# Optimization experiments

Measured on AMD Instinct MI355X. Metric: run time of the kernel, lower is better.

## Reference

```python
import jax, jax.numpy as jnp
import numpy as np

# Straight-through deterministic binarization (sign), identity grad —
# matches the .data in-place Binarize trick in BinaryNet.pytorch.
@jax.custom_vjp
def binarize(x):
    return jnp.sign(x)
def _bin_fwd(x):
    return jnp.sign(x), None
def _bin_bwd(res, g):
    return (g,)
binarize.defvjp(_bin_fwd, _bin_bwd)

# Stochastic binary activation: p = hard_sigmoid(x), out = 2*Bernoulli(p)-1,
# straight-through estimator gated on |x|<=1.
@jax.custom_vjp
def stoch_act(x, u):
    p = jnp.clip((x + 1.0) * 0.5, 0.0, 1.0)
    return jnp.where(u < p, 1.0, -1.0).astype(x.dtype)
def _sa_fwd(x, u):
    p = jnp.clip((x + 1.0) * 0.5, 0.0, 1.0)
    return jnp.where(u < p, 1.0, -1.0).astype(x.dtype), x
def _sa_bwd(x, g):
    return (g * (jnp.abs(x) <= 1.0).astype(g.dtype), jnp.zeros(x.shape, g.dtype))
stoch_act.defvjp(_sa_fwd, _sa_bwd)

def bconv(x, w, b, bin_in):
    # BinarizeConv2d: binarize input unless it has 3 channels; always binarize weight
    xi = binarize(x) if bin_in else x
    y = jax.lax.conv_general_dilated(
        xi, binarize(w), window_strides=(1, 1), padding=((1, 1), (1, 1)),
        dimension_numbers=('NCHW', 'OIHW', 'NCHW'))
    return y + b[None, :, None, None]

def blin(x, w, b):
    # BinarizeLinear: input dim != 784 so input is binarized; weight binarized
    return binarize(x) @ binarize(w).T + b

def _forward(x, w1, b1, w2, b2, w3, b3, w4, b4, w5, b5, w6, b6, fw1, fb1, fw2, fb2, fw3, fb3):
    keys = jax.random.split(jax.random.key(42), 9)
    def act(h, i):
        return stoch_act(h, jax.random.uniform(keys[i], h.shape, h.dtype))
    h = act(bconv(x, w1, b1, False), 0)          # [B,128,32,32]
    h = act(bconv(h, w2, b2, True), 1)           # [B,256,32,32]
    h = act(bconv(h, w3, b3, True), 2)
    h = act(bconv(h, w4, b4, True), 3)
    h = act(bconv(h, w5, b5, True), 4)           # [B,512,32,32]
    h = act(bconv(h, w6, b6, True), 5)
    h = h.reshape(-1, 512 * 4 * 4)               # faithful view(-1, 8192) -> [64*B, 8192]
    h = act(blin(h, fw1, fb1), 6)
    h = act(blin(h, fw2, fb2), 7)
    h = act(blin(h, fw3, fb3), 8)                # [64*B, 10]
    return h

def setup_inputs():
    key = jax.random.key(0)
    ks = jax.random.split(key, 20)
    n = lambda k, s: jax.random.normal(k, s, jnp.float32)
    return {
        'x': n(ks[0], (64, 3, 32, 32)),
        'w1': n(ks[1], (128, 3, 3, 3)) * 0.1, 'b1': n(ks[2], (128,)) * 0.1,
        'w2': n(ks[3], (256, 128, 3, 3)) * 0.1, 'b2': n(ks[4], (256,)) * 0.1,
        'w3': n(ks[5], (256, 256, 3, 3)) * 0.1, 'b3': n(ks[6], (256,)) * 0.1,
        'w4': n(ks[7], (256, 256, 3, 3)) * 0.1, 'b4': n(ks[8], (256,)) * 0.1,
        'w5': n(ks[9], (512, 256, 3, 3)) * 0.1, 'b5': n(ks[10], (512,)) * 0.1,
        'w6': n(ks[11], (512, 512, 3, 3)) * 0.1, 'b6': n(ks[12], (512,)) * 0.1,
        'fw1': n(ks[13], (1024, 8192)) * 0.02, 'fb1': n(ks[14], (1024,)) * 0.02,
        'fw2': n(ks[15], (1024, 1024)) * 0.02, 'fb2': n(ks[16], (1024,)) * 0.02,
        'fw3': n(ks[17], (10, 1024)) * 0.02, 'fb3': n(ks[18], (10,)) * 0.02,
    }

def reference(x, w1, b1, w2, b2, w3, b3, w4, b4, w5, b5, w6, b6, fw1, fb1, fw2, fb2, fw3, fb3):
    return _forward(x, w1, b1, w2, b2, w3, b3, w4, b4, w5, b5, w6, b6, fw1, fb1, fw2, fb2, fw3, fb3)
```

## Files before the change

### kernel.cpp

```cpp
#include <hip/hip_runtime.h>
#include <stdint.h>

typedef unsigned int u32;
typedef unsigned long long u64;
typedef int v4i __attribute__((ext_vector_type(4)));
typedef int v16i __attribute__((ext_vector_type(16)));

__host__ __device__ __forceinline__ void tf2x32(u32 k0, u32 k1, u32 x0, u32 x1,
                                                u32& o0, u32& o1) {
  u32 k2 = k0 ^ k1 ^ 0x1BD11BDAu;
  x0 += k0; x1 += k1;
#ifdef __HIP_DEVICE_COMPILE__
#define ROTL(v, r) __builtin_rotateleft32((v), (r))
#else
#define ROTL(v, r) (((v) << (r)) | ((v) >> (32 - (r))))
#endif
#define TFR(r) { x0 += x1; x1 = ROTL(x1, r); x1 ^= x0; }
  TFR(13) TFR(15) TFR(26) TFR(6)   x0 += k1; x1 += k2 + 1u;
  TFR(17) TFR(29) TFR(16) TFR(24)  x0 += k2; x1 += k0 + 2u;
  TFR(13) TFR(15) TFR(26) TFR(6)   x0 += k0; x1 += k1 + 3u;
  TFR(17) TFR(29) TFR(16) TFR(24)  x0 += k1; x1 += k2 + 4u;
  TFR(13) TFR(15) TFR(26) TFR(6)   x0 += k2; x1 += k0 + 5u;
#undef TFR
#undef ROTL
  o0 = x0; o1 = x1;
}

__device__ __forceinline__ bool act_neg(float y, u32 k0, u32 k1, u32 j) {
  u32 o0, o1;
  tf2x32(k0, k1, 0u, j, o0, o1);
  u32 bits = o0 ^ o1;
  float uf = __uint_as_float(0x3f800000u | (bits >> 9));
  float u2 = __builtin_fmaf(uf, 2.0f, -2.0f);
  float t1 = y + 1.0f;
  return !(u2 < t1);
}

__global__ void k_pack_wfrag(const float* __restrict__ w, u32* __restrict__ bf,
                             int Cout, int Cin) {
  const int W = Cin >> 5;
  const int total = (Cout >> 5) * W * 9 * 256;
  int idx = blockIdx.x * blockDim.x + threadIdx.x;
  if (idx >= total) return;
  int i4 = idx & 3;
  int l = (idx >> 2) & 63;
  int t = (idx >> 8) % 9;
  int kt = (idx / 2304) % W;
  int cot = idx / (2304 * W);
  int co = cot * 32 + (l & 31);
  int ci0 = kt * 32 + (l >> 5) * 16 + i4 * 4;
  int kh = t / 3, kw = t % 3;
  u32 v = 0;
#pragma unroll
  for (int b = 0; b < 4; ++b) {
    float wf = w[((size_t)(co * Cin + ci0 + b) * 3 + kh) * 3 + kw];
    v |= (wf < 0.0f ? 0xFFu : 0x01u) << (8 * b);
  }
  bf[idx] = v;
}

__global__ void k_pack_fcwT(const float* __restrict__ w, u32* __restrict__ pwT,
                            int O, int K) {
  int KW = K >> 5;
  int idx = blockIdx.x * blockDim.x + threadIdx.x;
  if (idx >= O * KW) return;
  int kw = idx % KW, o = idx / KW;
  const float4* src = (const float4*)(w + (size_t)o * K + kw * 32);
  u32 word = 0;
#pragma unroll
  for (int b4 = 0; b4 < 8; ++b4) {
    float4 f = src[b4];
    word |= (f.x < 0.0f ? 1u : 0u) << (b4 * 4 + 0);
    word |= (f.y < 0.0f ? 1u : 0u) << (b4 * 4 + 1);
    word |= (f.z < 0.0f ? 1u : 0u) << (b4 * 4 + 2);
    word |= (f.w < 0.0f ? 1u : 0u) << (b4 * 4 + 3);
  }
  int k4 = kw >> 2, j = kw & 3;
  pwT[((size_t)k4 * O + o) * 4 + j] = word;
}

__global__ void k_pack_fcw(const float* __restrict__ w, u32* __restrict__ pw,
                           int O, int K) {
  int KW = K >> 5;
  int idx = blockIdx.x * blockDim.x + threadIdx.x;
  if (idx >= O * KW) return;
  int kw = idx % KW, o = idx / KW;
  const float4* src = (const float4*)(w + (size_t)o * K + kw * 32);
  u32 word = 0;
#pragma unroll
  for (int b4 = 0; b4 < 8; ++b4) {
    float4 f = src[b4];
    word |= (f.x < 0.0f ? 1u : 0u) << (b4 * 4 + 0);
    word |= (f.y < 0.0f ? 1u : 0u) << (b4 * 4 + 1);
    word |= (f.z < 0.0f ? 1u : 0u) << (b4 * 4 + 2);
    word |= (f.w < 0.0f ? 1u : 0u) << (b4 * 4 + 3);
  }
  pw[idx] = word;
}

__global__ __launch_bounds__(256) void k_conv1(
    const float* __restrict__ x, const float* __restrict__ w1,
    const float* __restrict__ b1, u32 k0, u32 k1, u32* __restrict__ out) {
  int wave = (blockIdx.x * 256 + threadIdx.x) >> 6;
  int lane = threadIdx.x & 63;
  int n = wave >> 10;
  int rem = wave & 1023;
  int y = rem >> 5, xx = rem & 31;

  float xv[27];
#pragma unroll
  for (int ci = 0; ci < 3; ++ci)
#pragma unroll
    for (int dy = -1; dy <= 1; ++dy)
#pragma unroll
      for (int dx = -1; dx <= 1; ++dx) {
        int gy = y + dy, gx = xx + dx;
        float v = 0.0f;
        if ((unsigned)gy < 32u && (unsigned)gx < 32u)
          v = x[((n * 3 + ci) * 32 + gy) * 32 + gx];
        xv[(ci * 3 + (dy + 1)) * 3 + (dx + 1)] = v;
      }

  u64 bm[2];
#pragma unroll
  for (int h = 0; h < 2; ++h) {
    int co = lane + h * 64;
    float acc = 0.0f;
#pragma unroll
    for (int kh = 0; kh < 3; ++kh)
#pragma unroll
      for (int kw = 0; kw < 3; ++kw)
#pragma unroll
        for (int ci = 0; ci < 3; ++ci) {
          int k = (ci * 3 + kh) * 3 + kw;
          float wv = w1[co * 27 + k];
          acc += (wv < 0.0f) ? -xv[k] : xv[k];
        }
    float yv = acc + b1[co];
    u32 j = ((u32)(n * 128 + co) << 10) | (u32)(y << 5) | (u32)xx;
    bm[h] = __ballot(act_neg(yv, k0, k1, j));
  }
  if (lane < 4) {
    u32 wsel = (lane & 1) ? (u32)(bm[lane >> 1] >> 32) : (u32)bm[lane >> 1];
    out[(u32)(n * 4 + lane) * 1024u + (u32)(y * 32 + xx)] = wsel;
  }
}

template <int W>
__global__ __launch_bounds__(512) void k_bconv11(
    const u32* __restrict__ in, const u32* __restrict__ bfrag,
    const float* __restrict__ bias, int Cout, u32 k0, u32 k1,
    u32* __restrict__ out) {
  const int tid = threadIdx.x;
  const int lane = tid & 63;
  const int wv = tid >> 6;
  const int n = blockIdx.x;
  const int y0 = blockIdx.y * 4;
  const int cot = blockIdx.z * 8 + wv;
  const int WOUT = Cout >> 5;

  __shared__ __align__(16) u32 sl[2][2][6 * 36 * 4];

  const int er = tid / 34;
  const int exc = tid % 34;
  const bool eact = tid < 204;
  const int egy = y0 - 1 + er;
  const int egx = exc - 1;
  const bool ein =
      eact && ((unsigned)egy < 32u) && ((unsigned)egx < 32u);

  v16i acc[4];
#pragma unroll
  for (int r = 0; r < 4; ++r)
#pragma unroll
    for (int e = 0; e < 16; ++e) acc[r][e] = 0;

  {
    u32 word = ein ? in[(u32)(n * W) * 1024u + (u32)(egy * 32 + egx)] : 0u;
    if (eact) {
#pragma unroll
      for (int h = 0; h < 2; ++h) {
        v4i v;
#pragma unroll
        for (int q = 0; q < 4; ++q) {
          u32 nib = (word >> ((4 * h + q) * 4)) & 0xFu;
          u32 spread = (nib * 0x00204081u) & 0x01010101u;
          u32 val = (spread * 0xFEu) ^ 0x01010101u;
          v[q] = ein ? (int)val : 0;
        }
        *(v4i*)&sl[0][h][(er * 36 + exc) * 4] = v;
      }
    }
  }
  __syncthreads();

#pragma unroll 1
  for (int kt = 0; kt < W; ++kt) {
    const int cur = kt & 1;
    u32 wn = 0;
    if (kt + 1 < W && ein)
      wn = in[(u32)(n * W + kt + 1) * 1024u + (u32)(egy * 32 + egx)];

    v4i af[18];
    const int xb = lane & 31;
    const u32* slc = sl[cur][lane >> 5];
#pragma unroll
    for (int sr = 0; sr < 6; ++sr)
#pragma unroll
      for (int dxx = 0; dxx < 3; ++dxx)
        af[sr * 3 + dxx] = *(const v4i*)&slc[(sr * 36 + xb + dxx) * 4];

    const u32* bptr = bfrag + ((size_t)(cot * W + kt) * 9) * 256 + lane * 4;
#pragma unroll
    for (int t = 0; t < 9; ++t) {
      v4i B = *(const v4i*)(bptr + t * 256);
      const int dy = t / 3 - 1, dxx = t % 3;
#pragma unroll
      for (int r = 0; r < 4; ++r)
        acc[r] = __builtin_amdgcn_mfma_i32_32x32x32_i8(
            af[(r + dy + 1) * 3 + dxx], B, acc[r], 0, 0, 0);
    }

    if (kt + 1 < W && eact) {
#pragma unroll
      for (int h = 0; h < 2; ++h) {
        v4i v;
#pragma unroll
        for (int q = 0; q < 4; ++q) {
          u32 nib = (wn >> ((4 * h + q) * 4)) & 0xFu;
          u32 spread = (nib * 0x00204081u) & 0x01010101u;
          u32 val = (spread * 0xFEu) ^ 0x01010101u;
          v[q] = ein ? (int)val : 0;
        }
        *(v4i*)&sl[cur ^ 1][h][(er * 36 + exc) * 4] = v;
      }
    }
    __syncthreads();
  }

  const int co = cot * 32 + (lane & 31);
  const float bo = bias[co];
  const u32 jb = (u32)(n * Cout + co) * 1024u;
  const u32 obase = (u32)(n * WOUT + cot) * 1024u + (u32)((lane >> 5) * 4);
#pragma unroll
  for (int r = 0; r < 4; ++r) {
    const int y = y0 + r;
#pragma unroll
    for (int reg = 0; reg < 16; ++reg) {
      const int mlo = (reg & 3) + 8 * (reg >> 2);
      const int m = mlo + 4 * (lane >> 5);
      float yv = (float)acc[r][reg] + bo;
      bool neg = act_neg(yv, k0, k1, jb + (u32)(y * 32 + m));
      u64 b = __ballot(neg);
      if ((lane & 31) == 0) {
        u32 vsel = (lane == 0) ? (u32)b : (u32)(b >> 32);
        out[obase + (u32)(y * 32 + mlo)] = vsel;
      }
    }
  }
}

__global__ void k_repack(const u32* __restrict__ a6, u32* __restrict__ f0) {
  int idx = blockIdx.x * blockDim.x + threadIdx.x;
  if (idx >= 4096 * 256) return;
  int w = idx & 255, r = idx >> 8;
  int n = r >> 6, chi = r & 63;
  int clo = w >> 5, yy = w & 31;
  int c = chi * 8 + clo;
  const u32* base = a6 + (u32)(n * 16 + (c >> 5)) * 1024u + (u32)(yy * 32);
  u32 sh = (u32)(c & 31);
  u32 word = 0;
#pragma unroll
  for (int xp = 0; xp < 32; ++xp)
    word |= ((base[xp] >> sh) & 1u) << xp;
  f0[idx] = word;
}

template <int KW>
__global__ __launch_bounds__(256, 4) void k_fct(
    const u32* __restrict__ in, const u32* __restrict__ pwT,
    const float* __restrict__ bias, int O, u32 k0, u32 k1,
    u32* __restrict__ out) {
  const int tid = threadIdx.x, lane = tid & 63;
  const int wv = __builtin_amdgcn_readfirstlane(tid >> 6);
  const int rbase = blockIdx.x * 32;
  const int obase = blockIdx.y * 64;
  __shared__ __align__(16) u32 rows[32 * KW];
  for (int i = tid; i < 32 * KW; i += 256)
    rows[i] = in[(size_t)(rbase + i / KW) * KW + (i % KW)];
  __syncthreads();

  const int o = obase + lane;
  const int r0 = wv * 8;
  u32 acc[8];
#pragma unroll
  for (int rr = 0; rr < 8; ++rr) acc[rr] = 0;
  for (int k4 = 0; k4 < KW / 4; ++k4) {
    uint4 w4 = ((const uint4*)pwT)[(size_t)k4 * O + o];
#pragma unroll
    for (int rr = 0; rr < 8; ++rr) {
      uint4 av = *(const uint4*)&rows[(r0 + rr) * KW + k4 * 4];
      acc[rr] += __popc(av.x ^ w4.x) + __popc(av.y ^ w4.y) +
                 __popc(av.z ^ w4.z) + __popc(av.w ^ w4.w);
    }
  }
  const int OW = O >> 5;
  const float bo = bias[o];
#pragma unroll
  for (int rr = 0; rr < 8; ++rr) {
    int r = rbase + r0 + rr;
    float yv = (float)(KW * 32 - 2 * (int)acc[rr]) + bo;
    bool neg = act_neg(yv, k0, k1, (u32)r * (u32)O + (u32)o);
    u64 b = __ballot(neg);
    if (lane == 0) {
      out[(size_t)r * OW + (obase >> 5)] = (u32)b;
      out[(size_t)r * OW + (obase >> 5) + 1] = (u32)(b >> 32);
    }
  }
}

__global__ __launch_bounds__(64) void k_fc3(
    const u32* __restrict__ in, const u32* __restrict__ pw,
    const float* __restrict__ bias, u32 k0, u32 k1,
    float* __restrict__ outp) {
  const int lane = threadIdx.x;
  const int r = blockIdx.x;
  __shared__ u32 row[32];
  if (lane < 32) row[lane] = in[(size_t)r * 32 + lane];
  __syncthreads();
  if (lane < 10) {
    int acc = 0;
#pragma unroll
    for (int k = 0; k < 32; ++k) acc += __popc(row[k] ^ pw[lane * 32 + k]);
    float yv = (float)(1024 - 2 * acc) + bias[lane];
    bool neg = act_neg(yv, k0, k1, (u32)r * 10u + (u32)lane);
    outp[(size_t)r * 10 + lane] = neg ? -1.0f : 1.0f;
  }
}

extern "C" void kernel_launch(void* const* d_in, const int* in_sizes, int n_in,
                              void* d_out, int out_size, void* d_ws,
                              size_t ws_size, hipStream_t stream) {
  const float* x   = (const float*)d_in[0];
  const float* w1  = (const float*)d_in[1];
  const float* b1  = (const float*)d_in[2];
  const float* w2  = (const float*)d_in[3];
  const float* b2  = (const float*)d_in[4];
  const float* w3  = (const float*)d_in[5];
  const float* b3  = (const float*)d_in[6];
  const float* w4  = (const float*)d_in[7];
  const float* b4  = (const float*)d_in[8];
  const float* w5  = (const float*)d_in[9];
  const float* b5  = (const float*)d_in[10];
  const float* w6  = (const float*)d_in[11];
  const float* b6  = (const float*)d_in[12];
  const float* fw1 = (const float*)d_in[13];
  const float* fb1 = (const float*)d_in[14];
  const float* fw2 = (const float*)d_in[15];
  const float* fb2 = (const float*)d_in[16];
  const float* fw3 = (const float*)d_in[17];
  const float* fb3 = (const float*)d_in[18];

  u32 K[9][2];
  for (int i = 0; i < 9; ++i) tf2x32(0u, 42u, 0u, (u32)i, K[i][0], K[i][1]);

  char* ws = (char*)d_ws;
  size_t off = 0;
  auto alloc = [&](size_t bytes) -> char* {
    char* p = ws + off;
    off += (bytes + 255) & ~(size_t)255;
    return p;
  };
  u32* bf2  = (u32*)alloc(256u * 9 * 128);
  u32* bf3  = (u32*)alloc(256u * 9 * 256);
  u32* bf4  = (u32*)alloc(256u * 9 * 256);
  u32* bf5  = (u32*)alloc(512u * 9 * 256);
  u32* bf6  = (u32*)alloc(512u * 9 * 512);
  u32* pfw1 = (u32*)alloc(1024u * 256 * 4);
  u32* pfw2 = (u32*)alloc(1024u * 32 * 4);
  u32* pfw3 = (u32*)alloc(10u * 32 * 4);
  u32* a1   = (u32*)alloc(64u * 1024 * 4 * 4);
  u32* a2   = (u32*)alloc(64u * 1024 * 8 * 4);
  u32* a3   = (u32*)alloc(64u * 1024 * 8 * 4);
  u32* a4   = (u32*)alloc(64u * 1024 * 8 * 4);
  u32* a5   = (u32*)alloc(64u * 1024 * 16 * 4);
  u32* a6   = (u32*)alloc(64u * 1024 * 16 * 4);
  u32* f0   = (u32*)alloc(4096u * 256 * 4);
  u32* f1   = (u32*)alloc(4096u * 32 * 4);
  u32* f2   = (u32*)alloc(4096u * 32 * 4);
  (void)ws_size;

  int t;
  t = (256 / 32) * 4 * 9 * 256;
  k_pack_wfrag<<<(t + 255) / 256, 256, 0, stream>>>(w2, bf2, 256, 128);
  t = (256 / 32) * 8 * 9 * 256;
  k_pack_wfrag<<<(t + 255) / 256, 256, 0, stream>>>(w3, bf3, 256, 256);
  k_pack_wfrag<<<(t + 255) / 256, 256, 0, stream>>>(w4, bf4, 256, 256);
  t = (512 / 32) * 8 * 9 * 256;
  k_pack_wfrag<<<(t + 255) / 256, 256, 0, stream>>>(w5, bf5, 512, 256);
  t = (512 / 32) * 16 * 9 * 256;
  k_pack_wfrag<<<(t + 255) / 256, 256, 0, stream>>>(w6, bf6, 512, 512);
  t = 1024 * 256;
  k_pack_fcwT<<<(t + 255) / 256, 256, 0, stream>>>(fw1, pfw1, 1024, 8192);
  t = 1024 * 32;
  k_pack_fcwT<<<(t + 255) / 256, 256, 0, stream>>>(fw2, pfw2, 1024, 1024);
  t = 10 * 32;
  k_pack_fcw<<<(t + 255) / 256, 256, 0, stream>>>(fw3, pfw3, 10, 1024);

  k_conv1<<<16384, 256, 0, stream>>>(x, w1, b1, K[0][0], K[0][1], a1);
  k_bconv11<4><<<dim3(64, 8, 1), 512, 0, stream>>>(a1, bf2, b2, 256,
                                                   K[1][0], K[1][1], a2);
  k_bconv11<8><<<dim3(64, 8, 1), 512, 0, stream>>>(a2, bf3, b3, 256,
                                                   K[2][0], K[2][1], a3);
  k_bconv11<8><<<dim3(64, 8, 1), 512, 0, stream>>>(a3, bf4, b4, 256,
                                                   K[3][0], K[3][1], a4);
  k_bconv11<8><<<dim3(64, 8, 2), 512, 0, stream>>>(a4, bf5, b5, 512,
                                                   K[4][0], K[4][1], a5);
  k_bconv11<16><<<dim3(64, 8, 2), 512, 0, stream>>>(a5, bf6, b6, 512,
                                                    K[5][0], K[5][1], a6);
  k_repack<<<(4096 * 256 + 255) / 256, 256, 0, stream>>>(a6, f0);
  k_fct<256><<<dim3(128, 16), 256, 0, stream>>>(f0, pfw1, fb1, 1024,
                                                K[6][0], K[6][1], f1);
  k_fct<32><<<dim3(128, 16), 256, 0, stream>>>(f1, pfw2, fb2, 1024,
                                               K[7][0], K[7][1], f2);
  k_fc3<<<4096, 64, 0, stream>>>(f2, pfw3, fb3, K[8][0], K[8][1],
                                 (float*)d_out);
}
```

Measured before the change: 647.1 us.

## Run FC1 on int8 MFMA and widen the Cout=512 conv blocks to 16 waves

Replaces the bitwise (popcount-style) FC1 kernel with an MFMA-based int8 GEMM. The FC1 weights are pre-packed into ±1 byte fragments and the activations are expanded from bits into ±1 bytes in double-buffered shared memory. The conv kernel is templated on wave count, so the two 512-channel layers run 1024-thread blocks covering all output tiles, instead of 512-thread blocks over two z-slices. This should cut FC1 compute and halve how often the input tiles are reloaded for the 512-channel convs. In exchange it packs an 8 MB weight buffer every call and runs larger blocks, which may lower occupancy.

```diff
diff --git a/kernel.cpp b/kernel.cpp
--- a/kernel.cpp
+++ b/kernel.cpp
@@ -59,6 +59,24 @@
   bf[idx] = v;
 }
 
+__global__ void k_pack_fcbf(const float* __restrict__ w, u32* __restrict__ bfc) {
+  int idx = blockIdx.x * blockDim.x + threadIdx.x;
+  if (idx >= 32 * 256 * 256) return;
+  int q = idx & 3;
+  int l = (idx >> 2) & 63;
+  int kt = (idx >> 8) & 255;
+  int ot = idx >> 16;
+  int o = ot * 32 + (l & 31);
+  int k0i = kt * 32 + (l >> 5) * 16 + q * 4;
+  u32 v = 0;
+#pragma unroll
+  for (int b = 0; b < 4; ++b) {
+    float wf = w[(size_t)o * 8192 + k0i + b];
+    v |= (wf < 0.0f ? 0xFFu : 0x01u) << (8 * b);
+  }
+  bfc[idx] = v;
+}
+
 __global__ void k_pack_fcwT(const float* __restrict__ w, u32* __restrict__ pwT,
                             int O, int K) {
   int KW = K >> 5;
@@ -146,8 +164,8 @@
   }
 }
 
-template <int W>
-__global__ __launch_bounds__(512) void k_bconv11(
+template <int W, int NW>
+__global__ __launch_bounds__(NW * 64) void k_bconv12(
     const u32* __restrict__ in, const u32* __restrict__ bfrag,
     const float* __restrict__ bias, int Cout, u32 k0, u32 k1,
     u32* __restrict__ out) {
@@ -156,7 +174,7 @@
   const int wv = tid >> 6;
   const int n = blockIdx.x;
   const int y0 = blockIdx.y * 4;
-  const int cot = blockIdx.z * 8 + wv;
+  const int cot = blockIdx.z * NW + wv;
   const int WOUT = Cout >> 5;
 
   __shared__ __align__(16) u32 sl[2][2][6 * 36 * 4];
@@ -241,7 +259,7 @@
   const int co = cot * 32 + (lane & 31);
   const float bo = bias[co];
   const u32 jb = (u32)(n * Cout + co) * 1024u;
-  const u32 obase = (u32)(n * WOUT + cot) * 1024u + (u32)((lane >> 5) * 4);
+  const u32 obase = (u32)(n * WOUT + cot) * 1024u;
 #pragma unroll
   for (int r = 0; r < 4; ++r) {
     const int y = y0 + r;
@@ -254,7 +272,7 @@
       u64 b = __ballot(neg);
       if ((lane & 31) == 0) {
         u32 vsel = (lane == 0) ? (u32)b : (u32)(b >> 32);
-        out[obase + (u32)(y * 32 + mlo)] = vsel;
+        out[obase + (u32)(y * 32 + mlo + (lane >> 5) * 4)] = vsel;
       }
     }
   }
@@ -274,6 +292,90 @@
   for (int xp = 0; xp < 32; ++xp)
     word |= ((base[xp] >> sh) & 1u) << xp;
   f0[idx] = word;
+}
+
+__global__ __launch_bounds__(512) void k_fcm(
+    const u32* __restrict__ f0, const u32* __restrict__ bfc,
+    const float* __restrict__ bias, u32 k0, u32 k1, u32* __restrict__ out) {
+  const int tid = threadIdx.x;
+  const int lane = tid & 63;
+  const int wv = tid >> 6;
+  const int rbase = blockIdx.x * 32;
+  const int ot = blockIdx.y * 8 + wv;
+  const int obase = ot * 32;
+
+  __shared__ __align__(16) u32 sl[2][8][2][32 * 4];
+
+  const int ikt = tid >> 5;
+  const int irow = tid & 31;
+  const bool eact = tid < 256;
+
+  v16i acc;
+#pragma unroll
+  for (int e = 0; e < 16; ++e) acc[e] = 0;
+
+  if (eact) {
+    u32 word = f0[(u32)(rbase + irow) * 256u + (u32)ikt];
+#pragma unroll
+    for (int h = 0; h < 2; ++h) {
+      v4i v;
+#pragma unroll
+      for (int q = 0; q < 4; ++q) {
+        u32 nib = (word >> ((4 * h + q) * 4)) & 0xFu;
+        u32 spread = (nib * 0x00204081u) & 0x01010101u;
+        v[q] = (int)((spread * 0xFEu) ^ 0x01010101u);
+      }
+      *(v4i*)&sl[0][ikt][h][irow * 4] = v;
+    }
+  }
+  __syncthreads();
+
+#pragma unroll 1
+  for (int ch = 0; ch < 32; ++ch) {
+    const int cur = ch & 1;
+    u32 wn = 0;
+    if (ch + 1 < 32 && eact)
+      wn = f0[(u32)(rbase + irow) * 256u + (u32)((ch + 1) * 8 + ikt)];
+
+    const u32* bptr = bfc + ((size_t)(ot * 256 + ch * 8)) * 256 + lane * 4;
+#pragma unroll
+    for (int k8 = 0; k8 < 8; ++k8) {
+      v4i A = *(const v4i*)&sl[cur][k8][lane >> 5][(lane & 31) * 4];
+      v4i B = *(const v4i*)(bptr + k8 * 256);
+      acc = __builtin_amdgcn_mfma_i32_32x32x32_i8(A, B, acc, 0, 0, 0);
+    }
+
+    if (ch + 1 < 32 && eact) {
+#pragma unroll
+      for (int h = 0; h < 2; ++h) {
+        v4i v;
+#pragma unroll
+        for (int q = 0; q < 4; ++q) {
+          u32 nib = (wn >> ((4 * h + q) * 4)) & 0xFu;
+          u32 spread = (nib * 0x00204081u) & 0x01010101u;
+          v[q] = (int)((spread * 0xFEu) ^ 0x01010101u);
+        }
+        *(v4i*)&sl[cur ^ 1][ikt][h][irow * 4] = v;
+      }
+    }
+    __syncthreads();
+  }
+
+  const int o = obase + (lane & 31);
+  const float bo = bias[o];
+#pragma unroll
+  for (int reg = 0; reg < 16; ++reg) {
+    const int rlo = (reg & 3) + 8 * (reg >> 2);
+    const int r = rbase + rlo + 4 * (lane >> 5);
+    float yv = (float)acc[reg] + bo;
+    bool neg = act_neg(yv, k0, k1, (u32)r * 1024u + (u32)o);
+    u64 b = __ballot(neg);
+    if ((lane & 31) == 0) {
+      u32 vsel = (lane == 0) ? (u32)b : (u32)(b >> 32);
+      int rw = rbase + rlo + (lane >> 5) * 4;
+      out[(size_t)rw * 32 + (u32)ot] = vsel;
+    }
+  }
 }
 
 template <int KW>
@@ -376,7 +478,7 @@
   u32* bf4  = (u32*)alloc(256u * 9 * 256);
   u32* bf5  = (u32*)alloc(512u * 9 * 256);
   u32* bf6  = (u32*)alloc(512u * 9 * 512);
-  u32* pfw1 = (u32*)alloc(1024u * 256 * 4);
+  u32* bfc1 = (u32*)alloc(1024u * 8192);
   u32* pfw2 = (u32*)alloc(1024u * 32 * 4);
   u32* pfw3 = (u32*)alloc(10u * 32 * 4);
   u32* a1   = (u32*)alloc(64u * 1024 * 4 * 4);
@@ -400,27 +502,26 @@
   k_pack_wfrag<<<(t + 255) / 256, 256, 0, stream>>>(w5, bf5, 512, 256);
   t = (512 / 32) * 16 * 9 * 256;
   k_pack_wfrag<<<(t + 255) / 256, 256, 0, stream>>>(w6, bf6, 512, 512);
-  t = 1024 * 256;
-  k_pack_fcwT<<<(t + 255) / 256, 256, 0, stream>>>(fw1, pfw1, 1024, 8192);
+  t = 32 * 256 * 256;
+  k_pack_fcbf<<<(t + 255) / 256, 256, 0, stream>>>(fw1, bfc1);
   t = 1024 * 32;
   k_pack_fcwT<<<(t + 255) / 256, 256, 0, stream>>>(fw2, pfw2, 1024, 1024);
   t = 10 * 32;
   k_pack_fcw<<<(t + 255) / 256, 256, 0, stream>>>(fw3, pfw3, 10, 1024);
 
   k_conv1<<<16384, 256, 0, stream>>>(x, w1, b1, K[0][0], K[0][1], a1);
-  k_bconv11<4><<<dim3(64, 8, 1), 512, 0, stream>>>(a1, bf2, b2, 256,
-                                                   K[1][0], K[1][1], a2);
-  k_bconv11<8><<<dim3(64, 8, 1), 512, 0, stream>>>(a2, bf3, b3, 256,
-                                                   K[2][0], K[2][1], a3);
-  k_bconv11<8><<<dim3(64, 8, 1), 512, 0, stream>>>(a3, bf4, b4, 256,
-                                                   K[3][0], K[3][1], a4);
-  k_bconv11<8><<<dim3(64, 8, 2), 512, 0, stream>>>(a4, bf5, b5, 512,
-                                                   K[4][0], K[4][1], a5);
-  k_bconv11<16><<<dim3(64, 8, 2), 512, 0, stream>>>(a5, bf6, b6, 512,
-                                                    K[5][0], K[5][1], a6);
+  k_bconv12<4, 8><<<dim3(64, 8, 1), 512, 0, stream>>>(a1, bf2, b2, 256,
+                                                      K[1][0], K[1][1], a2);
+  k_bconv12<8, 8><<<dim3(64, 8, 1), 512, 0, stream>>>(a2, bf3, b3, 256,
+                                                      K[2][0], K[2][1], a3);
+  k_bconv12<8, 8><<<dim3(64, 8, 1), 512, 0, stream>>>(a3, bf4, b4, 256,
+                                                      K[3][0], K[3][1], a4);
+  k_bconv12<8, 16><<<dim3(64, 8, 1), 1024, 0, stream>>>(a4, bf5, b5, 512,
+                                                        K[4][0], K[4][1], a5);
+  k_bconv12<16, 16><<<dim3(64, 8, 1), 1024, 0, stream>>>(a5, bf6, b6, 512,
+                                                         K[5][0], K[5][1], a6);
   k_repack<<<(4096 * 256 + 255) / 256, 256, 0, stream>>>(a6, f0);
-  k_fct<256><<<dim3(128, 16), 256, 0, stream>>>(f0, pfw1, fb1, 1024,
-                                                K[6][0], K[6][1], f1);
+  k_fcm<<<dim3(128, 4), 512, 0, stream>>>(f0, bfc1, fb1, K[6][0], K[6][1], f1);
   k_fct<32><<<dim3(128, 16), 256, 0, stream>>>(f1, pfw2, fb2, 1024,
                                                K[7][0], K[7][1], f2);
   k_fc3<<<4096, 64, 0, stream>>>(f2, pfw3, fb3, K[8][0], K[8][1],
```

New measurement: 652.1 us. Within noise of the previous version (+0.8%).
